# Kernel optimization log

Measured on AMD Instinct MI355X. Metric: run time of the kernel, lower is better.

## Reference

```python
import jax, jax.numpy as jnp
import numpy as np

S, B, H, D, G = 2048, 2, 16, 128, 16  # seq, batch, heads, head_dim, v-quant groups


def setup_inputs() -> dict:
    key = jax.random.key(0)
    ks = jax.random.split(key, 9)
    # int8-valued activations stored as float (torch code does .to(torch.int8))
    q = jax.random.randint(ks[0], (S, B, H, D), -128, 128).astype(jnp.float32)
    k = jax.random.randint(ks[1], (S, B, H, D), -128, 128).astype(jnp.float32)
    v = jax.random.randint(ks[2], (S, B, H, D), -128, 128).astype(jnp.float32)
    qmin = jax.random.normal(ks[3], (S, B, H, 1), jnp.float32) * 0.01
    qscale = jax.random.uniform(ks[4], (S, B, H, 1), jnp.float32, 0.005, 0.02)
    kmin = jax.random.normal(ks[5], (S, B, H, 1), jnp.float32) * 0.01
    kscale = jax.random.uniform(ks[6], (S, B, H, 1), jnp.float32, 0.005, 0.02)
    vmin = jax.random.normal(ks[7], (G, B, H, D, 1), jnp.float32) * 0.01
    vscale = jax.random.uniform(ks[8], (G, B, H, D, 1), jnp.float32, 0.005, 0.02)
    return {"query_layer": q, "key_layer": k, "value_layer": v,
            "qmin": qmin, "qscale": qscale, "kmin": kmin, "kscale": kscale,
            "vmin": vmin, "vscale": vscale, "causal": 1}


def _attention(query_layer, key_layer, value_layer, qmin, qscale, kmin, kscale, vmin, vscale, causal):
    # s b h d -> b h s d ; emulate .to(torch.int8) (values are already int8-range ints)
    q = jnp.transpose(query_layer, (1, 2, 0, 3))
    k = jnp.transpose(key_layer, (1, 2, 0, 3))
    v = jnp.transpose(value_layer, (1, 2, 0, 3))
    # per-token quant factors: s b h 1 -> b h s 1
    qm = jnp.transpose(qmin[..., 0], (1, 2, 0))[..., None]
    qs = jnp.transpose(qscale[..., 0], (1, 2, 0))[..., None]
    km = jnp.transpose(kmin[..., 0], (1, 2, 0))[..., None]
    ksc = jnp.transpose(kscale[..., 0], (1, 2, 0))[..., None]
    # attnq_qk: dequantize per-token then QK^T
    qd = q * qs + qm
    kd = k * ksc + km
    scores = jnp.einsum('bhsd,bhtd->bhst', qd, kd)
    # softmaxq: scale by 1/sqrt(128), causal mask, softmax, int8 requant of probs
    scores = scores * jnp.float32(1.0 / np.sqrt(128.0))
    s = scores.shape[-1]
    if causal:
        mask = jnp.tril(jnp.ones((s, s), dtype=bool))
        scores = jnp.where(mask, scores, jnp.float32(-1e9))
    probs = jax.nn.softmax(scores, axis=-1)
    pmin = jnp.min(probs, axis=-1, keepdims=True)
    pmax = jnp.max(probs, axis=-1, keepdims=True)
    pscale = (pmax - pmin) / 255.0 + jnp.float32(1e-12)
    quant_prob = jnp.round((probs - pmin) / pscale)  # int8-range prob codes
    # attnq_pv: dequant probs (per query token) and V (per sequence group) then PV
    pd = quant_prob * pscale + pmin
    vm = jnp.transpose(vmin[..., 0], (1, 2, 0, 3))  # b h g d
    vs = jnp.transpose(vscale[..., 0], (1, 2, 0, 3))
    gs = v.shape[2] // vm.shape[2]  # group size along sequence
    vd = v * jnp.repeat(vs, gs, axis=2) + jnp.repeat(vm, gs, axis=2)
    out = jnp.einsum('bhst,bhtd->bhsd', pd, vd)
    b, h, sq, d = out.shape
    return jnp.transpose(out, (2, 0, 1, 3)).reshape(sq, b, h * d)  # s b (h d)


def reference(query_layer, key_layer, value_layer, qmin, qscale, kmin, kscale, vmin, vscale, causal):
    return _attention(query_layer, key_layer, value_layer, qmin, qscale, kmin, kscale, vmin, vscale, causal)
```

## Files before the change

kernel.cpp:

```cpp
#include <hip/hip_runtime.h>
#include <math.h>


#define S_LEN 2048
#define BATCH 2
#define NH    16
#define HD    128
#define RSTR  4096
#define SCALE2 (0.08838834764831845f * 1.4426950408889634f)
#define EXP2F(x) __builtin_amdgcn_exp2f(x)

typedef int v4i __attribute__((ext_vector_type(4)));
#define MFMA16(a,b,c) __builtin_amdgcn_mfma_i32_16x16x64_i8((a),(b),(c),0,0,0)

#define WS_K8   0u
#define WS_V8T  (8u*1024u*1024u)
#define WS_SQ   (16u*1024u*1024u)
#define WS_SK   (WS_SQ + 256u*1024u)
#define WS_GSV  (WS_SK + 256u*1024u)
#define WS_VSUM (WS_GSV + 256u*1024u)

__global__ __launch_bounds__(256) void prep_sums(
    const float* __restrict__ Q, const float* __restrict__ K,
    signed char* __restrict__ K8, float* __restrict__ SQs, float* __restrict__ SKs)
{
    int idx = blockIdx.x*256 + threadIdx.x;
    int tensor = blockIdx.y;
    const float* src = tensor ? K : Q;
    int tau = idx >> 5, dg = idx & 31;
    float4 x = *(const float4*)(src + (size_t)tau*128 + 4*dg);
    float ssum = x.x + x.y + x.z + x.w;
    #pragma unroll
    for (int off = 16; off >= 1; off >>= 1) ssum += __shfl_xor(ssum, off);
    if (tensor) {
        int a=(int)x.x, b2=(int)x.y, c=(int)x.z, d=(int)x.w;
        ((int*)K8)[(size_t)tau*32 + dg] = (a&255)|((b2&255)<<8)|((c&255)<<16)|((d&255)<<24);
        if ((threadIdx.x & 31) == 0) SKs[tau] = ssum;
    } else {
        if ((threadIdx.x & 31) == 0) SQs[tau] = ssum;
    }
}

__device__ __forceinline__ int sbsum(unsigned p) {
    return (int)(signed char)(p) + (int)(signed char)(p>>8)
         + (int)(signed char)(p>>16) + (int)(signed char)(p>>24);
}

__global__ __launch_bounds__(256) void prep_v(
    const float* __restrict__ V, signed char* __restrict__ V8T, float* __restrict__ GSV)
{
    __shared__ int v8i[128*33];
    int tid = threadIdx.x;
    int bh = blockIdx.x & 31, ck = blockIdx.x >> 5;
    int b = bh >> 4, h = bh & 15;
    int t0 = ck * 128;
    int boff = b*2048 + h*128;
    #pragma unroll
    for (int it = 0; it < 16; ++it) {
        int idx = tid + it*256;
        int t = idx >> 5, dw = idx & 31;
        float4 x = *(const float4*)(V + (size_t)(t0+t)*RSTR + boff + 4*dw);
        int a=(int)x.x, b2=(int)x.y, c=(int)x.z, d=(int)x.w;
        v8i[t*33 + dw] = (a&255)|((b2&255)<<8)|((c&255)<<16)|((d&255)<<24);
    }
    __syncthreads();
    #pragma unroll
    for (int it = 0; it < 4; ++it) {
        int j = tid + it*256;
        int tg = j & 31, dw = j >> 5;
        unsigned r0 = (unsigned)v8i[(4*tg+0)*33 + dw];
        unsigned r1 = (unsigned)v8i[(4*tg+1)*33 + dw];
        unsigned r2 = (unsigned)v8i[(4*tg+2)*33 + dw];
        unsigned r3 = (unsigned)v8i[(4*tg+3)*33 + dw];
        unsigned x01 = __builtin_amdgcn_perm(r1, r0, 0x05010400u);
        unsigned x23 = __builtin_amdgcn_perm(r3, r2, 0x05010400u);
        unsigned y01 = __builtin_amdgcn_perm(r1, r0, 0x07030602u);
        unsigned y23 = __builtin_amdgcn_perm(r3, r2, 0x07030602u);
        unsigned p[4];
        p[0] = __builtin_amdgcn_perm(x23, x01, 0x05040100u);
        p[1] = __builtin_amdgcn_perm(x23, x01, 0x07060302u);
        p[2] = __builtin_amdgcn_perm(y23, y01, 0x05040100u);
        p[3] = __builtin_amdgcn_perm(y23, y01, 0x07060302u);
        int s[4];
        #pragma unroll
        for (int jj = 0; jj < 4; ++jj) {
            int d = 4*dw + jj;
            *(int*)(V8T + ((size_t)bh*128 + d)*2048 + t0 + 4*tg) = (int)p[jj];
            s[jj] = sbsum(p[jj]);
        }
        #pragma unroll
        for (int off = 1; off < 32; off <<= 1) {
            #pragma unroll
            for (int jj = 0; jj < 4; ++jj) s[jj] += __shfl_xor(s[jj], off);
        }
        if (tg == 0) {
            #pragma unroll
            for (int jj = 0; jj < 4; ++jj)
                GSV[((size_t)bh*16 + ck)*128 + 4*dw + jj] = (float)s[jj];
        }
    }
}

__global__ __launch_bounds__(256) void prep_vsum(
    const float* __restrict__ GSV, const float* __restrict__ VSC,
    const float* __restrict__ VMN, float* __restrict__ VSUM)
{
    int idx = blockIdx.x*256 + threadIdx.x;
    int bh = idx >> 7, d = idx & 127;
    int b = bh >> 4, h = bh & 15;
    float acc = 0.f;
    for (int g = 0; g < 16; ++g) {
        float gs = GSV[((size_t)bh*16 + g)*128 + d];
        int vi = ((g*BATCH + b)*NH + h)*HD + d;
        acc = fmaf(VSC[vi], gs, fmaf(128.0f, VMN[vi], acc));
    }
    VSUM[bh*128 + d] = acc;
}

__global__ __launch_bounds__(256, 2) void attn_main(
    const float* __restrict__ Q,
    const signed char* __restrict__ K8, const signed char* __restrict__ V8T,
    const float* __restrict__ QMN, const float* __restrict__ QSC,
    const float* __restrict__ KMN, const float* __restrict__ KSC,
    const float* __restrict__ VMN, const float* __restrict__ VSC,
    const float* __restrict__ SQs, const float* __restrict__ SKs,
    const float* __restrict__ GSV, const float* __restrict__ VSUM,
    const int* __restrict__ CAUSAL, float* __restrict__ OUT)
{
    __shared__ __align__(16) signed char q8s[64*144];
    __shared__ __align__(16) signed char k8s[128*144];
    __shared__ __align__(16) signed char v8s[128*144];
    __shared__ __align__(16) signed char pcs[64*144];
    __shared__ float rs_c1[64], rs_c2[64], rs_c3[64];
    __shared__ float rs_mx[64], rs_den[64], rs_mn[64];
    __shared__ float rs_u1[64], rs_w1[64], rs_psc[64], rs_pmn[64];
    __shared__ float ktA[128], ktB[128], ktC[128];
    __shared__ float vsA[128], vsB[128], vsC[128];

    const int tid  = threadIdx.x;
    const int w    = tid >> 6;
    const int lane = tid & 63;
    const int n    = lane & 15;
    const int quad = lane >> 4;
    const int bhi  = blockIdx.x & 31;
    const int qt   = 31 - (int)(blockIdx.x >> 5);
    const int b    = bhi >> 4, h = bhi & 15;
    const int causal = *CAUSAL;
    const int s0   = qt * 64;
    const int boff = b*2048 + h*128;
    const v4i vzero = {0,0,0,0};
    const v4i ones  = {0x01010101,0x01010101,0x01010101,0x01010101};

    #pragma unroll
    for (int it = 0; it < 8; ++it) {
        int idx = tid + it*256;
        int row = idx >> 5, d4 = (idx & 31) << 2;
        float4 x = *(const float4*)(Q + (size_t)(s0+row)*RSTR + boff + d4);
        int a=(int)x.x, b2=(int)x.y, c=(int)x.z, d=(int)x.w;
        *(int*)(q8s + row*144 + d4) = (a&255)|((b2&255)<<8)|((c&255)<<16)|((d&255)<<24);
    }
    if (tid < 64) {
        int si = (s0 + tid)*32 + bhi;
        float qs = QSC[si], qm = QMN[si];
        rs_c1[tid] = qs; rs_c2[tid] = qm;
        rs_c3[tid] = fmaf(qs, SQs[si], 128.0f*qm);
    }
    __syncthreads();

    const int kt_end = causal ? ((s0 + 63) >> 7) : 15;

    float c1r[4], c2r[4], c3r[4]; int qgr[4];
    #pragma unroll
    for (int r = 0; r < 4; ++r) {
        int qq = 16*w + 4*quad + r;
        c1r[r] = rs_c1[qq]; c2r[r] = rs_c2[qq]; c3r[r] = rs_c3[qq];
        qgr[r] = s0 + qq;
    }
    v4i a0p = *(const v4i*)(q8s + (16*w + n)*144 + 16*quad);
    v4i a1p = *(const v4i*)(q8s + (16*w + n)*144 + 64 + 16*quad);

    float m[4], l[4], mn[4];
    #pragma unroll
    for (int r = 0; r < 4; ++r) { m[r] = -INFINITY; l[r] = 0.f; mn[r] = INFINITY; }

#define P1_TILE(MASKED)                                                          \
  do {                                                                           \
    const int t0g = kt * 128;                                                    \
    __syncthreads();                                                             \
    _Pragma("unroll")                                                            \
    for (int it = 0; it < 4; ++it) {                                             \
        int idx = tid + it*256;                                                  \
        int trow = idx >> 3, doff = (idx & 7) << 4;                              \
        *(uint4*)(k8s + trow*144 + doff) =                                       \
            *(const uint4*)(K8 + ((size_t)(t0g+trow)*32 + bhi)*128 + doff);      \
    }                                                                            \
    if (tid < 128) {                                                             \
        int si = (t0g + tid)*32 + bhi;                                           \
        ktA[tid] = KSC[si]*SCALE2; ktB[tid] = KMN[si]*SCALE2; ktC[tid] = SKs[si];\
    }                                                                            \
    __syncthreads();                                                             \
    float tmax[4], sarr[8][4];                                                   \
    _Pragma("unroll")                                                            \
    for (int r = 0; r < 4; ++r) tmax[r] = -INFINITY;                             \
    _Pragma("unroll")                                                            \
    for (int tb = 0; tb < 8; ++tb) {                                             \
        v4i b0 = *(const v4i*)(k8s + (16*tb + n)*144 + 16*quad);                 \
        v4i b1 = *(const v4i*)(k8s + (16*tb + n)*144 + 64 + 16*quad);            \
        v4i acc = MFMA16(a0p, b0, vzero);                                        \
        acc = MFMA16(a1p, b1, acc);                                              \
        int tl = 16*tb + n;                                                      \
        float ks = ktA[tl], km = ktB[tl], sk = ktC[tl];                          \
        _Pragma("unroll")                                                        \
        for (int r = 0; r < 4; ++r) {                                            \
            float Sf = (float)acc[r];                                            \
            float sv = fmaf(ks, fmaf(c1r[r], Sf, c2r[r]*sk), km*c3r[r]);         \
            if (MASKED) sv = (t0g + tl > qgr[r]) ? -INFINITY : sv;               \
            sarr[tb][r] = sv;                                                    \
            tmax[r] = fmaxf(tmax[r], sv);                                        \
            mn[r] = fminf(mn[r], sv);                                            \
        }                                                                        \
    }                                                                            \
    _Pragma("unroll")                                                            \
    for (int r = 0; r < 4; ++r) {                                                \
        float mm = fmaxf(m[r], tmax[r]);                                         \
        if (mm > -INFINITY) {                                                    \
            float a2 = l[r]*EXP2F(m[r]-mm);                                      \
            _Pragma("unroll")                                                    \
            for (int tb = 0; tb < 8; ++tb) a2 += EXP2F(sarr[tb][r]-mm);          \
            l[r] = a2; m[r] = mm;                                                \
        }                                                                        \
    }                                                                            \
  } while (0)

    {
        int kt;
        for (kt = 0; kt < kt_end; ++kt) P1_TILE(false);
        kt = kt_end;
        if (causal) P1_TILE(true); else P1_TILE(false);
    }

    #pragma unroll
    for (int r = 0; r < 4; ++r) {
        #pragma unroll
        for (int off = 1; off < 16; off <<= 1) {
            float m2 = __shfl_xor(m[r], off);
            float l2 = __shfl_xor(l[r], off);
            float n2 = __shfl_xor(mn[r], off);
            float mm = fmaxf(m[r], m2);
            if (mm > -INFINITY) l[r] = l[r]*EXP2F(m[r]-mm) + l2*EXP2F(m2-mm);
            m[r] = mm;
            mn[r] = fminf(mn[r], n2);
        }
        if (n == 0) {
            int qq = 16*w + 4*quad + r;
            rs_mx[qq] = m[r]; rs_den[qq] = l[r]; rs_mn[qq] = mn[r];
        }
    }
    __syncthreads();
    if (tid < 64) {
        float mx = rs_mx[tid], den = rs_den[tid], mnv = rs_mn[tid];
        float invd = 1.0f/den;
        int s = s0 + tid;
        bool hasmask = (causal != 0) && (s < S_LEN-1);
        float pmin = hasmask ? 0.0f : EXP2F(mnv - mx)*invd;
        float psc  = (invd - pmin)/255.0f + 1e-12f;
        float ipsc = 1.0f/psc;
        rs_u1[tid] = invd*ipsc; rs_w1[tid] = -pmin*ipsc;
        rs_psc[tid] = psc; rs_pmn[tid] = pmin;
    }

    float outa[4][8];
    #pragma unroll
    for (int r = 0; r < 4; ++r)
        #pragma unroll
        for (int db = 0; db < 8; ++db) outa[r][db] = 0.f;

#define P2_TILE(MASKED)                                                          \
  do {                                                                           \
    const int t0g = kt * 128;                                                    \
    __syncthreads();                                                             \
    _Pragma("unroll")                                                            \
    for (int it = 0; it < 4; ++it) {                                             \
        int idx = tid + it*256;                                                  \
        int trow = idx >> 3, doff = (idx & 7) << 4;                              \
        *(uint4*)(k8s + trow*144 + doff) =                                       \
            *(const uint4*)(K8 + ((size_t)(t0g+trow)*32 + bhi)*128 + doff);      \
        *(uint4*)(v8s + trow*144 + doff) =                                       \
            *(const uint4*)(V8T + ((size_t)bhi*128 + trow)*2048 + t0g + doff);   \
    }                                                                            \
    if (tid < 128) {                                                             \
        int si = (t0g + tid)*32 + bhi;                                           \
        ktA[tid] = KSC[si]*SCALE2; ktB[tid] = KMN[si]*SCALE2; ktC[tid] = SKs[si];\
    } else {                                                                     \
        int d = tid - 128;                                                       \
        int vi = ((kt*BATCH + b)*NH + h)*HD + d;                                 \
        float vs = VSC[vi], vm = VMN[vi];                                        \
        float gs = GSV[((size_t)bhi*16 + kt)*128 + d];                           \
        vsA[d] = vs; vsB[d] = vm;                                                \
        vsC[d] = fmaf(128.0f*vs, gs, 16384.0f*vm);                               \
    }                                                                            \
    __syncthreads();                                                             \
    _Pragma("unroll")                                                            \
    for (int rb = 0; rb < 2; ++rb) {                                             \
        int trow = 32*w + 16*rb;                                                 \
        v4i a0 = *(const v4i*)(k8s + (trow + n)*144 + 16*quad);                  \
        v4i a1 = *(const v4i*)(k8s + (trow + n)*144 + 64 + 16*quad);             \
        float ksr[4], kmr[4], skr[4];                                            \
        int tgb = t0g + trow + 4*quad;                                           \
        _Pragma("unroll")                                                        \
        for (int r = 0; r < 4; ++r) {                                            \
            int tl = trow + 4*quad + r;                                          \
            ksr[r] = ktA[tl]; kmr[r] = ktB[tl]; skr[r] = ktC[tl];                \
        }                                                                        \
        _Pragma("unroll")                                                        \
        for (int cb = 0; cb < 4; ++cb) {                                         \
            v4i b0 = *(const v4i*)(q8s + (16*cb + n)*144 + 16*quad);             \
            v4i b1 = *(const v4i*)(q8s + (16*cb + n)*144 + 64 + 16*quad);        \
            v4i acc = MFMA16(a0, b0, vzero);                                     \
            acc = MFMA16(a1, b1, acc);                                           \
            int qcol = 16*cb + n, qg = s0 + qcol;                                \
            float c1 = rs_c1[qcol], c2 = rs_c2[qcol], c3 = rs_c3[qcol];          \
            float mxq = rs_mx[qcol], u1 = rs_u1[qcol], w1 = rs_w1[qcol];         \
            int packed = 0;                                                      \
            _Pragma("unroll")                                                    \
            for (int r = 0; r < 4; ++r) {                                        \
                float Sf = (float)acc[r];                                        \
                float x = fmaf(ksr[r], fmaf(c1, Sf, c2*skr[r]),                  \
                               fmaf(kmr[r], c3, -mxq));                          \
                if (MASKED) x = (tgb + r > qg) ? -INFINITY : x;                  \
                float e = EXP2F(x);                                              \
                int ci = (int)rintf(fmaf(e, u1, w1));                            \
                packed |= ci << (8*r);                                           \
            }                                                                    \
            packed ^= 0x80808080;                       \
            *(int*)(pcs + qcol*144 + trow + 4*quad) = packed;                    \
        }                                                                        \
    }                                                                            \
    __syncthreads();                                                             \
    {                                                                            \
        v4i a0 = *(const v4i*)(pcs + (16*w + n)*144 + 16*quad);                  \
        v4i a1 = *(const v4i*)(pcs + (16*w + n)*144 + 64 + 16*quad);             \
        v4i c1a = MFMA16(a0, ones, vzero);                                       \
        c1a = MFMA16(a1, ones, c1a);                                             \
        float c1f[4];                                                            \
        _Pragma("unroll")                                                        \
        for (int r = 0; r < 4; ++r) c1f[r] = (float)c1a[r];                      \
        _Pragma("unroll")                                                        \
        for (int db = 0; db < 8; ++db) {                                         \
            v4i b0 = *(const v4i*)(v8s + (16*db + n)*144 + 16*quad);             \
            v4i b1 = *(const v4i*)(v8s + (16*db + n)*144 + 64 + 16*quad);        \
            v4i cv = MFMA16(a0, b0, vzero);                                      \
            cv = MFMA16(a1, b1, cv);                                             \
            int d = 16*db + n;                                                   \
            float vs = vsA[d], vm = vsB[d], Bd = vsC[d];                         \
            _Pragma("unroll")                                                    \
            for (int r = 0; r < 4; ++r)                                          \
                outa[r][db] = fmaf(vs, (float)cv[r],                             \
                                   fmaf(vm, c1f[r], outa[r][db] + Bd));          \
        }                                                                        \
    }                                                                            \
  } while (0)

    {
        int kt;
        for (kt = 0; kt < kt_end; ++kt) P2_TILE(false);
        kt = kt_end;
        if (causal) P2_TILE(true); else P2_TILE(false);
    }

    float pscr[4], pmnr[4];
    #pragma unroll
    for (int r = 0; r < 4; ++r) {
        int qq = 16*w + 4*quad + r;
        pscr[r] = rs_psc[qq]; pmnr[r] = rs_pmn[qq];
    }
    #pragma unroll
    for (int db = 0; db < 8; ++db) {
        int d = 16*db + n;
        float vsum = VSUM[bhi*128 + d];
        #pragma unroll
        for (int r = 0; r < 4; ++r) {
            int s = s0 + 16*w + 4*quad + r;
            OUT[(size_t)s*RSTR + boff + d] = fmaf(pscr[r], outa[r][db], pmnr[r]*vsum);
        }
    }
}

extern "C" void kernel_launch(void* const* d_in, const int* in_sizes, int n_in,
                              void* d_out, int out_size, void* d_ws, size_t ws_size,
                              hipStream_t stream) {
    (void)in_sizes; (void)n_in; (void)out_size; (void)ws_size;
    const float* Q   = (const float*)d_in[0];
    const float* K   = (const float*)d_in[1];
    const float* V   = (const float*)d_in[2];
    const float* QMN = (const float*)d_in[3];
    const float* QSC = (const float*)d_in[4];
    const float* KMN = (const float*)d_in[5];
    const float* KSC = (const float*)d_in[6];
    const float* VMN = (const float*)d_in[7];
    const float* VSC = (const float*)d_in[8];
    const int*   CS  = (const int*)d_in[9];
    float* out = (float*)d_out;

    char* ws = (char*)d_ws;
    signed char* K8  = (signed char*)(ws + WS_K8);
    signed char* V8T = (signed char*)(ws + WS_V8T);
    float* SQs  = (float*)(ws + WS_SQ);
    float* SKs  = (float*)(ws + WS_SK);
    float* GSVp = (float*)(ws + WS_GSV);
    float* VSUM = (float*)(ws + WS_VSUM);

    prep_sums<<<dim3(8192, 2), 256, 0, stream>>>(Q, K, K8, SQs, SKs);
    prep_v<<<512, 256, 0, stream>>>(V, V8T, GSVp);
    prep_vsum<<<16, 256, 0, stream>>>(GSVp, VSC, VMN, VSUM);
    attn_main<<<1024, 256, 0, stream>>>(Q, K8, V8T, QMN, QSC, KMN, KSC, VMN, VSC,
                                        SQs, SKs, GSVp, VSUM, CS, out);
}
```

Before: 263.9 us.

## Merge prep kernels, hoist Q fragments, stream K from global, fold V bias

Merges the three prep kernels into one launch and moves the per-column V-sum computation into the attention kernel prologue. The per-tile V bias term is summed once per column and added at the end instead of on every tile. In pass 2, Q fragments and per-row softmax constants are hoisted into registers, and K is read from global memory instead of being staged in LDS. The probability-quantisation rounding uses a float magic-number trick with byte-perm packing, and the exp sum is reassociated into a tree. Direct global K reads may raise latency, and the extra registers may pressure occupancy.

```diff
diff --git a/kernel.cpp b/kernel.cpp
--- a/kernel.cpp
+++ b/kernel.cpp
@@ -18,103 +18,87 @@
 #define WS_SQ   (16u*1024u*1024u)
 #define WS_SK   (WS_SQ + 256u*1024u)
 #define WS_GSV  (WS_SK + 256u*1024u)
-#define WS_VSUM (WS_GSV + 256u*1024u)
-
-__global__ __launch_bounds__(256) void prep_sums(
-    const float* __restrict__ Q, const float* __restrict__ K,
-    signed char* __restrict__ K8, float* __restrict__ SQs, float* __restrict__ SKs)
-{
-    int idx = blockIdx.x*256 + threadIdx.x;
-    int tensor = blockIdx.y;
-    const float* src = tensor ? K : Q;
-    int tau = idx >> 5, dg = idx & 31;
-    float4 x = *(const float4*)(src + (size_t)tau*128 + 4*dg);
-    float ssum = x.x + x.y + x.z + x.w;
-    #pragma unroll
-    for (int off = 16; off >= 1; off >>= 1) ssum += __shfl_xor(ssum, off);
-    if (tensor) {
-        int a=(int)x.x, b2=(int)x.y, c=(int)x.z, d=(int)x.w;
-        ((int*)K8)[(size_t)tau*32 + dg] = (a&255)|((b2&255)<<8)|((c&255)<<16)|((d&255)<<24);
-        if ((threadIdx.x & 31) == 0) SKs[tau] = ssum;
-    } else {
-        if ((threadIdx.x & 31) == 0) SQs[tau] = ssum;
-    }
-}
 
 __device__ __forceinline__ int sbsum(unsigned p) {
     return (int)(signed char)(p) + (int)(signed char)(p>>8)
          + (int)(signed char)(p>>16) + (int)(signed char)(p>>24);
 }
 
-__global__ __launch_bounds__(256) void prep_v(
-    const float* __restrict__ V, signed char* __restrict__ V8T, float* __restrict__ GSV)
+__global__ __launch_bounds__(256) void prep_pack(
+    const float* __restrict__ Q, const float* __restrict__ K, const float* __restrict__ V,
+    signed char* __restrict__ K8, float* __restrict__ SQs, float* __restrict__ SKs,
+    signed char* __restrict__ V8T, float* __restrict__ GSV)
 {
     __shared__ int v8i[128*33];
-    int tid = threadIdx.x;
-    int bh = blockIdx.x & 31, ck = blockIdx.x >> 5;
-    int b = bh >> 4, h = bh & 15;
-    int t0 = ck * 128;
-    int boff = b*2048 + h*128;
-    #pragma unroll
-    for (int it = 0; it < 16; ++it) {
-        int idx = tid + it*256;
-        int t = idx >> 5, dw = idx & 31;
-        float4 x = *(const float4*)(V + (size_t)(t0+t)*RSTR + boff + 4*dw);
-        int a=(int)x.x, b2=(int)x.y, c=(int)x.z, d=(int)x.w;
-        v8i[t*33 + dw] = (a&255)|((b2&255)<<8)|((c&255)<<16)|((d&255)<<24);
-    }
-    __syncthreads();
-    #pragma unroll
-    for (int it = 0; it < 4; ++it) {
-        int j = tid + it*256;
-        int tg = j & 31, dw = j >> 5;
-        unsigned r0 = (unsigned)v8i[(4*tg+0)*33 + dw];
-        unsigned r1 = (unsigned)v8i[(4*tg+1)*33 + dw];
-        unsigned r2 = (unsigned)v8i[(4*tg+2)*33 + dw];
-        unsigned r3 = (unsigned)v8i[(4*tg+3)*33 + dw];
-        unsigned x01 = __builtin_amdgcn_perm(r1, r0, 0x05010400u);
-        unsigned x23 = __builtin_amdgcn_perm(r3, r2, 0x05010400u);
-        unsigned y01 = __builtin_amdgcn_perm(r1, r0, 0x07030602u);
-        unsigned y23 = __builtin_amdgcn_perm(r3, r2, 0x07030602u);
-        unsigned p[4];
-        p[0] = __builtin_amdgcn_perm(x23, x01, 0x05040100u);
-        p[1] = __builtin_amdgcn_perm(x23, x01, 0x07060302u);
-        p[2] = __builtin_amdgcn_perm(y23, y01, 0x05040100u);
-        p[3] = __builtin_amdgcn_perm(y23, y01, 0x07060302u);
-        int s[4];
-        #pragma unroll
-        for (int jj = 0; jj < 4; ++jj) {
-            int d = 4*dw + jj;
-            *(int*)(V8T + ((size_t)bh*128 + d)*2048 + t0 + 4*tg) = (int)p[jj];
-            s[jj] = sbsum(p[jj]);
-        }
-        #pragma unroll
-        for (int off = 1; off < 32; off <<= 1) {
+    const int tid = threadIdx.x;
+    const int bx  = blockIdx.x;
+    if (bx < 16384) {
+        const int tensor = bx >> 13;
+        const int idx = (bx & 8191)*256 + tid;
+        const float* src = tensor ? K : Q;
+        int tau = idx >> 5, dg = idx & 31;
+        float4 x = *(const float4*)(src + (size_t)tau*128 + 4*dg);
+        float ssum = x.x + x.y + x.z + x.w;
+        #pragma unroll
+        for (int off = 16; off >= 1; off >>= 1) ssum += __shfl_xor(ssum, off);
+        if (tensor) {
+            int a=(int)x.x, b2=(int)x.y, c=(int)x.z, d=(int)x.w;
+            ((int*)K8)[(size_t)tau*32 + dg] = (a&255)|((b2&255)<<8)|((c&255)<<16)|((d&255)<<24);
+            if ((tid & 31) == 0) SKs[tau] = ssum;
+        } else {
+            if ((tid & 31) == 0) SQs[tau] = ssum;
+        }
+    } else {
+        const int bid = bx - 16384;
+        const int bh = bid & 31, ck = bid >> 5;
+        const int b = bh >> 4, h = bh & 15;
+        const int t0 = ck * 128;
+        const int boff = b*2048 + h*128;
+        #pragma unroll
+        for (int it = 0; it < 16; ++it) {
+            int idx = tid + it*256;
+            int t = idx >> 5, dw = idx & 31;
+            float4 x = *(const float4*)(V + (size_t)(t0+t)*RSTR + boff + 4*dw);
+            int a=(int)x.x, b2=(int)x.y, c=(int)x.z, d=(int)x.w;
+            v8i[t*33 + dw] = (a&255)|((b2&255)<<8)|((c&255)<<16)|((d&255)<<24);
+        }
+        __syncthreads();
+        #pragma unroll
+        for (int it = 0; it < 4; ++it) {
+            int j = tid + it*256;
+            int tg = j & 31, dw = j >> 5;
+            unsigned r0 = (unsigned)v8i[(4*tg+0)*33 + dw];
+            unsigned r1 = (unsigned)v8i[(4*tg+1)*33 + dw];
+            unsigned r2 = (unsigned)v8i[(4*tg+2)*33 + dw];
+            unsigned r3 = (unsigned)v8i[(4*tg+3)*33 + dw];
+            unsigned x01 = __builtin_amdgcn_perm(r1, r0, 0x05010400u);
+            unsigned x23 = __builtin_amdgcn_perm(r3, r2, 0x05010400u);
+            unsigned y01 = __builtin_amdgcn_perm(r1, r0, 0x07030602u);
+            unsigned y23 = __builtin_amdgcn_perm(r3, r2, 0x07030602u);
+            unsigned p[4];
+            p[0] = __builtin_amdgcn_perm(x23, x01, 0x05040100u);
+            p[1] = __builtin_amdgcn_perm(x23, x01, 0x07060302u);
+            p[2] = __builtin_amdgcn_perm(y23, y01, 0x05040100u);
+            p[3] = __builtin_amdgcn_perm(y23, y01, 0x07060302u);
+            int s[4];
             #pragma unroll
-            for (int jj = 0; jj < 4; ++jj) s[jj] += __shfl_xor(s[jj], off);
-        }
-        if (tg == 0) {
+            for (int jj = 0; jj < 4; ++jj) {
+                int d = 4*dw + jj;
+                *(int*)(V8T + ((size_t)bh*128 + d)*2048 + t0 + 4*tg) = (int)p[jj];
+                s[jj] = sbsum(p[jj]);
+            }
             #pragma unroll
-            for (int jj = 0; jj < 4; ++jj)
-                GSV[((size_t)bh*16 + ck)*128 + 4*dw + jj] = (float)s[jj];
-        }
-    }
-}
-
-__global__ __launch_bounds__(256) void prep_vsum(
-    const float* __restrict__ GSV, const float* __restrict__ VSC,
-    const float* __restrict__ VMN, float* __restrict__ VSUM)
-{
-    int idx = blockIdx.x*256 + threadIdx.x;
-    int bh = idx >> 7, d = idx & 127;
-    int b = bh >> 4, h = bh & 15;
-    float acc = 0.f;
-    for (int g = 0; g < 16; ++g) {
-        float gs = GSV[((size_t)bh*16 + g)*128 + d];
-        int vi = ((g*BATCH + b)*NH + h)*HD + d;
-        acc = fmaf(VSC[vi], gs, fmaf(128.0f, VMN[vi], acc));
-    }
-    VSUM[bh*128 + d] = acc;
+            for (int off = 1; off < 32; off <<= 1) {
+                #pragma unroll
+                for (int jj = 0; jj < 4; ++jj) s[jj] += __shfl_xor(s[jj], off);
+            }
+            if (tg == 0) {
+                #pragma unroll
+                for (int jj = 0; jj < 4; ++jj)
+                    GSV[((size_t)bh*16 + ck)*128 + 4*dw + jj] = (float)s[jj];
+            }
+        }
+    }
 }
 
 __global__ __launch_bounds__(256, 2) void attn_main(
@@ -124,7 +108,7 @@
     const float* __restrict__ KMN, const float* __restrict__ KSC,
     const float* __restrict__ VMN, const float* __restrict__ VSC,
     const float* __restrict__ SQs, const float* __restrict__ SKs,
-    const float* __restrict__ GSV, const float* __restrict__ VSUM,
+    const float* __restrict__ GSV,
     const int* __restrict__ CAUSAL, float* __restrict__ OUT)
 {
     __shared__ __align__(16) signed char q8s[64*144];
@@ -135,7 +119,8 @@
     __shared__ float rs_mx[64], rs_den[64], rs_mn[64];
     __shared__ float rs_u1[64], rs_w1[64], rs_psc[64], rs_pmn[64];
     __shared__ float ktA[128], ktB[128], ktC[128];
-    __shared__ float vsA[128], vsB[128], vsC[128];
+    __shared__ float vsA[128], vsB[128];
+    __shared__ float vsumL[128], cgsL[128];
 
     const int tid  = threadIdx.x;
     const int w    = tid >> 6;
@@ -209,11 +194,11 @@
         v4i acc = MFMA16(a0p, b0, vzero);                                        \
         acc = MFMA16(a1p, b1, acc);                                              \
         int tl = 16*tb + n;                                                      \
-        float ks = ktA[tl], km = ktB[tl], sk = ktC[tl];                          \
+        float kA = ktA[tl], kB = ktB[tl], kC = ktC[tl];                          \
         _Pragma("unroll")                                                        \
         for (int r = 0; r < 4; ++r) {                                            \
             float Sf = (float)acc[r];                                            \
-            float sv = fmaf(ks, fmaf(c1r[r], Sf, c2r[r]*sk), km*c3r[r]);         \
+            float sv = fmaf(kA, fmaf(c1r[r], Sf, c2r[r]*kC), kB*c3r[r]);         \
             if (MASKED) sv = (t0g + tl > qgr[r]) ? -INFINITY : sv;               \
             sarr[tb][r] = sv;                                                    \
             tmax[r] = fmaxf(tmax[r], sv);                                        \
@@ -224,10 +209,12 @@
     for (int r = 0; r < 4; ++r) {                                                \
         float mm = fmaxf(m[r], tmax[r]);                                         \
         if (mm > -INFINITY) {                                                    \
-            float a2 = l[r]*EXP2F(m[r]-mm);                                      \
-            _Pragma("unroll")                                                    \
-            for (int tb = 0; tb < 8; ++tb) a2 += EXP2F(sarr[tb][r]-mm);          \
-            l[r] = a2; m[r] = mm;                                                \
+            float e0 = EXP2F(sarr[0][r]-mm) + EXP2F(sarr[1][r]-mm);              \
+            float e1 = EXP2F(sarr[2][r]-mm) + EXP2F(sarr[3][r]-mm);              \
+            float e2 = EXP2F(sarr[4][r]-mm) + EXP2F(sarr[5][r]-mm);              \
+            float e3 = EXP2F(sarr[6][r]-mm) + EXP2F(sarr[7][r]-mm);              \
+            l[r] = fmaf(l[r], EXP2F(m[r]-mm), (e0+e1)+(e2+e3));                  \
+            m[r] = mm;                                                           \
         }                                                                        \
     }                                                                            \
   } while (0)
@@ -267,6 +254,32 @@
         float ipsc = 1.0f/psc;
         rs_u1[tid] = invd*ipsc; rs_w1[tid] = -pmin*ipsc;
         rs_psc[tid] = psc; rs_pmn[tid] = pmin;
+    } else if (tid >= 128) {
+        int d = tid - 128;
+        float vsum = 0.f, cgs = 0.f;
+        #pragma unroll
+        for (int g = 0; g < 16; ++g) {
+            float gs = GSV[((size_t)bhi*16 + g)*128 + d];
+            int vi = ((g*BATCH + b)*NH + h)*HD + d;
+            float vs = VSC[vi], vm = VMN[vi];
+            vsum = fmaf(vs, gs, fmaf(128.0f, vm, vsum));
+            if (g <= kt_end) cgs = fmaf(128.0f*vs, gs, fmaf(16384.0f, vm, cgs));
+        }
+        vsumL[d] = vsum; cgsL[d] = cgs;
+    }
+    __syncthreads();
+
+    v4i qb0[4], qb1[4];
+    float qc1[4], qc2[4], qc3[4], qmxn[4], qu1[4], qw1[4];
+    int qgq[4];
+    #pragma unroll
+    for (int cb = 0; cb < 4; ++cb) {
+        int qcol = 16*cb + n;
+        qb0[cb] = *(const v4i*)(q8s + qcol*144 + 16*quad);
+        qb1[cb] = *(const v4i*)(q8s + qcol*144 + 64 + 16*quad);
+        qc1[cb] = rs_c1[qcol]; qc2[cb] = rs_c2[qcol]; qc3[cb] = rs_c3[qcol];
+        qmxn[cb] = -rs_mx[qcol]; qu1[cb] = rs_u1[qcol]; qw1[cb] = rs_w1[qcol];
+        qgq[cb] = s0 + qcol;
     }
 
     float outa[4][8];
@@ -278,13 +291,11 @@
 #define P2_TILE(MASKED)                                                          \
   do {                                                                           \
     const int t0g = kt * 128;                                                    \
-    __syncthreads();                                                             \
+    __syncthreads();                      \
     _Pragma("unroll")                                                            \
     for (int it = 0; it < 4; ++it) {                                             \
         int idx = tid + it*256;                                                  \
         int trow = idx >> 3, doff = (idx & 7) << 4;                              \
-        *(uint4*)(k8s + trow*144 + doff) =                                       \
-            *(const uint4*)(K8 + ((size_t)(t0g+trow)*32 + bhi)*128 + doff);      \
         *(uint4*)(v8s + trow*144 + doff) =                                       \
             *(const uint4*)(V8T + ((size_t)bhi*128 + trow)*2048 + t0g + doff);   \
     }                                                                            \
@@ -294,17 +305,16 @@
     } else {                                                                     \
         int d = tid - 128;                                                       \
         int vi = ((kt*BATCH + b)*NH + h)*HD + d;                                 \
-        float vs = VSC[vi], vm = VMN[vi];                                        \
-        float gs = GSV[((size_t)bhi*16 + kt)*128 + d];                           \
-        vsA[d] = vs; vsB[d] = vm;                                                \
-        vsC[d] = fmaf(128.0f*vs, gs, 16384.0f*vm);                               \
+        vsA[d] = VSC[vi]; vsB[d] = VMN[vi];                                      \
     }                                                                            \
     __syncthreads();                                                             \
     _Pragma("unroll")                                                            \
     for (int rb = 0; rb < 2; ++rb) {                                             \
         int trow = 32*w + 16*rb;                                                 \
-        v4i a0 = *(const v4i*)(k8s + (trow + n)*144 + 16*quad);                  \
-        v4i a1 = *(const v4i*)(k8s + (trow + n)*144 + 64 + 16*quad);             \
+        const signed char* kp = K8 + ((size_t)(t0g+trow+n)*32 + bhi)*128         \
+                                   + 16*quad;                                    \
+        v4i a0 = *(const v4i*)kp;              \
+        v4i a1 = *(const v4i*)(kp + 64);                                         \
         float ksr[4], kmr[4], skr[4];                                            \
         int tgb = t0g + trow + 4*quad;                                           \
         _Pragma("unroll")                                                        \
@@ -314,26 +324,26 @@
         }                                                                        \
         _Pragma("unroll")                                                        \
         for (int cb = 0; cb < 4; ++cb) {                                         \
-            v4i b0 = *(const v4i*)(q8s + (16*cb + n)*144 + 16*quad);             \
-            v4i b1 = *(const v4i*)(q8s + (16*cb + n)*144 + 64 + 16*quad);        \
-            v4i acc = MFMA16(a0, b0, vzero);                                     \
-            acc = MFMA16(a1, b1, acc);                                           \
-            int qcol = 16*cb + n, qg = s0 + qcol;                                \
-            float c1 = rs_c1[qcol], c2 = rs_c2[qcol], c3 = rs_c3[qcol];          \
-            float mxq = rs_mx[qcol], u1 = rs_u1[qcol], w1 = rs_w1[qcol];         \
-            int packed = 0;                                                      \
+            v4i acc = MFMA16(a0, qb0[cb], vzero);                                \
+            acc = MFMA16(a1, qb1[cb], acc);                                      \
+            int cby[4];                                                          \
             _Pragma("unroll")                                                    \
             for (int r = 0; r < 4; ++r) {                                        \
                 float Sf = (float)acc[r];                                        \
-                float x = fmaf(ksr[r], fmaf(c1, Sf, c2*skr[r]),                  \
-                               fmaf(kmr[r], c3, -mxq));                          \
-                if (MASKED) x = (tgb + r > qg) ? -INFINITY : x;                  \
+                float x = fmaf(ksr[r], fmaf(qc1[cb], Sf, qc2[cb]*skr[r]),        \
+                               fmaf(kmr[r], qc3[cb], qmxn[cb]));                 \
+                if (MASKED) x = (tgb + r > qgq[cb]) ? -INFINITY : x;             \
                 float e = EXP2F(x);                                              \
-                int ci = (int)rintf(fmaf(e, u1, w1));                            \
-                packed |= ci << (8*r);                                           \
+                float f = fmaf(e, qu1[cb], qw1[cb]) + 8388608.0f;   \
+                cby[r] = __float_as_int(f);                                      \
             }                                                                    \
-            packed ^= 0x80808080;                       \
-            *(int*)(pcs + qcol*144 + trow + 4*quad) = packed;                    \
+            unsigned t01 = __builtin_amdgcn_perm((unsigned)cby[1],               \
+                                                 (unsigned)cby[0], 0x00000400u); \
+            unsigned t23 = __builtin_amdgcn_perm((unsigned)cby[3],               \
+                                                 (unsigned)cby[2], 0x04000000u); \
+            int packed = (int)(__builtin_amdgcn_perm(t23, t01, 0x07060100u)      \
+                               ^ 0x80808080u);          \
+            *(int*)(pcs + (16*cb + n)*144 + trow + 4*quad) = packed;             \
         }                                                                        \
     }                                                                            \
     __syncthreads();                                                             \
@@ -352,11 +362,11 @@
             v4i cv = MFMA16(a0, b0, vzero);                                      \
             cv = MFMA16(a1, b1, cv);                                             \
             int d = 16*db + n;                                                   \
-            float vs = vsA[d], vm = vsB[d], Bd = vsC[d];                         \
+            float vs = vsA[d], vm = vsB[d];                                      \
             _Pragma("unroll")                                                    \
             for (int r = 0; r < 4; ++r)                                          \
                 outa[r][db] = fmaf(vs, (float)cv[r],                             \
-                                   fmaf(vm, c1f[r], outa[r][db] + Bd));          \
+                                   fmaf(vm, c1f[r], outa[r][db]));               \
         }                                                                        \
     }                                                                            \
   } while (0)
@@ -377,11 +387,12 @@
     #pragma unroll
     for (int db = 0; db < 8; ++db) {
         int d = 16*db + n;
-        float vsum = VSUM[bhi*128 + d];
+        float vsum = vsumL[d];
+        float cgs  = cgsL[d];
         #pragma unroll
         for (int r = 0; r < 4; ++r) {
             int s = s0 + 16*w + 4*quad + r;
-            OUT[(size_t)s*RSTR + boff + d] = fmaf(pscr[r], outa[r][db], pmnr[r]*vsum);
+            OUT[(size_t)s*RSTR + boff + d] = fmaf(pscr[r], outa[r][db] + cgs, pmnr[r]*vsum);
         }
     }
 }
@@ -408,11 +419,8 @@
     float* SQs  = (float*)(ws + WS_SQ);
     float* SKs  = (float*)(ws + WS_SK);
     float* GSVp = (float*)(ws + WS_GSV);
-    float* VSUM = (float*)(ws + WS_VSUM);
-
-    prep_sums<<<dim3(8192, 2), 256, 0, stream>>>(Q, K, K8, SQs, SKs);
-    prep_v<<<512, 256, 0, stream>>>(V, V8T, GSVp);
-    prep_vsum<<<16, 256, 0, stream>>>(GSVp, VSC, VMN, VSUM);
+
+    prep_pack<<<16384 + 512, 256, 0, stream>>>(Q, K, V, K8, SQs, SKs, V8T, GSVp);
     attn_main<<<1024, 256, 0, stream>>>(Q, K8, V8T, QMN, QSC, KMN, KSC, VMN, VSC,
-                                        SQs, SKs, GSVp, VSUM, CS, out);
+                                        SQs, SKs, GSVp, CS, out);
 }
```

After: 251.9 us. 4.5% less time.
